# Performance work log

Hardware: AMD Instinct MI355X
Metric: run time of the kernel (lower is better)

The kernel has to match this reference:

```python
import jax, jax.numpy as jnp
import numpy as np

N_USERS = 100000
N_ITEMS = 50000
D = 64
N_LAYERS = 3
E_RAW = 2_000_000
B = 4096


def setup_inputs() -> dict:
    rng = np.random.RandomState(0)
    u = rng.randint(0, N_USERS, E_RAW).astype(np.int64)
    i = rng.randint(0, N_ITEMS, E_RAW).astype(np.int64)
    lin = np.unique(u * N_ITEMS + i)  # dedupe interactions like the dok_matrix would
    u = (lin // N_ITEMS).astype(np.int32)
    i = (lin % N_ITEMS).astype(np.int32)
    deg_u = np.bincount(u, minlength=N_USERS).astype(np.float64)
    deg_i = np.bincount(i, minlength=N_ITEMS).astype(np.float64)
    inv_u = np.where(deg_u > 0, 1.0 / np.sqrt(np.maximum(deg_u, 1.0)), 0.0)
    inv_i = np.where(deg_i > 0, 1.0 / np.sqrt(np.maximum(deg_i, 1.0)), 0.0)
    val = (inv_u[u] * inv_i[i]).astype(np.float32)  # D^-1/2 A D^-1/2 entries
    # symmetric bipartite Laplacian: user block rows then item block rows
    rows = np.concatenate([u, i + N_USERS]).astype(np.int32)
    cols = np.concatenate([i + N_USERS, u]).astype(np.int32)
    vals = np.concatenate([val, val])

    key = jax.random.key(0)
    k1, k2, k3, k4 = jax.random.split(key, 4)
    embeds = jax.random.normal(k1, (N_USERS + N_ITEMS, D), jnp.float32) * 0.1
    users = jax.random.randint(k2, (B,), 0, N_USERS)
    pos_items = jax.random.randint(k3, (B,), 0, N_ITEMS)
    neg_items = jax.random.randint(k4, (B,), 0, N_ITEMS)
    return dict(embeds=embeds, vals=jnp.asarray(vals), rows=jnp.asarray(rows),
                cols=jnp.asarray(cols), users=users, pos_items=pos_items,
                neg_items=neg_items)


def reference(embeds, vals, rows, cols, users, pos_items, neg_items):
    N = N_USERS + N_ITEMS
    cur = embeds
    acc = embeds  # running sum over layer embeddings (incl. layer 0)
    for _ in range(N_LAYERS):
        msg = vals[:, None] * cur[cols]                      # [nnz, D] gather
        cur = jax.ops.segment_sum(msg, rows, num_segments=N)  # SpMM scatter-add
        acc = acc + cur
    mean = acc / (N_LAYERS + 1)
    user_e = mean[:N_USERS]
    item_e = mean[N_USERS:]
    return user_e[users], item_e[pos_items], item_e[neg_items]
```

## Files before the change

### kernel.cpp

```cpp
#include <hip/hip_runtime.h>
#include <hip/hip_bf16.h>

#define N_USERS 100000
#define N_ITEMS 50000
#define N_TOT   150000
#define D       64
#define NBUCK   ((N_ITEMS + 255) >> 8)
#define BCAP    12288
#define CONVU_B 391
#define FLAG_B  48
#define SCAT_K  32

typedef float v2f __attribute__((ext_vector_type(2)));

__device__ __forceinline__ unsigned bf16rn(float f) {
    unsigned x = __float_as_uint(f);
    return (x + 0x7FFFu + ((x >> 16) & 1u)) >> 16;
}
__device__ __forceinline__ unsigned packbf(float a, float b) {
    return bf16rn(a) | (bf16rn(b) << 16);
}
__device__ __forceinline__ int lower_bound(const int* __restrict__ a, int n, int key) {
    int lo = 0, hi = n;
    while (lo < hi) {
        int mid = (lo + hi) >> 1;
        if (a[mid] < key) lo = mid + 1; else hi = mid;
    }
    return lo;
}

__global__ __launch_bounds__(256) void preA_kernel(
        const float* __restrict__ embeds, const int* __restrict__ rows,
        const int* __restrict__ cols, int* __restrict__ user_ptr,
        unsigned* __restrict__ ebfS, float* __restrict__ invrow,
        const int* __restrict__ users, const int* __restrict__ pos,
        const int* __restrict__ neg, unsigned char* __restrict__ flags,
        int* __restrict__ ccur, int* __restrict__ tmp,
        unsigned short* __restrict__ cols16, int E, int B) {
    int b = blockIdx.x, t = threadIdx.x;
    if (b < CONVU_B) {
        __shared__ int ptr_s[257];
        __shared__ float inv_s[256];
        int base = b * 256;
        int r = base + t;
        int v = lower_bound(rows, E, r);
        ptr_s[t] = v;
        if (r <= N_USERS) user_ptr[r] = v;
        if (t == 0) ptr_s[256] = lower_bound(rows, E, base + 256);
        __syncthreads();
        if (r < N_USERS) {
            int deg = ptr_s[t + 1] - ptr_s[t];
            float inv = (deg > 0) ? (float)(1.0 / sqrt((double)deg)) : 0.f;
            inv_s[t] = inv;
            invrow[r] = inv;
        } else inv_s[t] = 0.f;
        __syncthreads();
        int fl = t & 15;
        #pragma unroll
        for (int i = 0; i < 16; ++i) {
            int lr = i * 16 + (t >> 4);
            int row = base + lr;
            if (row < N_USERS) {
                float inv = inv_s[lr];
                float4 v4 = *(const float4*)(embeds + (size_t)row * D + fl * 4);
                uint2 o;
                o.x = packbf(inv * v4.x, inv * v4.y);
                o.y = packbf(inv * v4.z, inv * v4.w);
                *(uint2*)(ebfS + (size_t)row * 32 + fl * 2) = o;
            }
        }
    } else if (b < CONVU_B + FLAG_B) {
        int k = (b - CONVU_B) * 256 + t;
        if (k < 3 * B) {
            int row;
            if (k < B)          row = users[k];
            else if (k < 2 * B) row = N_USERS + pos[k - B];
            else                row = N_USERS + neg[k - 2 * B];
            flags[row] = 1;
        }
    } else {
        __shared__ int ebuf[256 * SCAT_K];
        __shared__ unsigned char bbuf[256 * SCAT_K];
        __shared__ int cnt[NBUCK];
        __shared__ int basep[NBUCK];
        int chunk = (b - CONVU_B - FLAG_B) * (256 * SCAT_K);
        if (t < NBUCK) cnt[t] = 0;
        __syncthreads();
        #pragma unroll 4
        for (int k = 0; k < SCAT_K; ++k) {
            int e = chunk + k * 256 + t;
            int idx = k * 256 + t;
            if (e < E) {
                int i = cols[e] - N_USERS;
                cols16[e] = (unsigned short)i;
                int bu = i >> 8;
                ebuf[idx] = ((i & 255) << 17) | rows[e];
                bbuf[idx] = (unsigned char)bu;
                atomicAdd(&cnt[bu], 1);
            } else bbuf[idx] = 255;
        }
        __syncthreads();
        if (t < NBUCK) {
            int c = cnt[t];
            basep[t] = c ? atomicAdd(&ccur[t], c) : 0;
            cnt[t] = 0;
        }
        __syncthreads();
        #pragma unroll 4
        for (int k = 0; k < SCAT_K; ++k) {
            int idx = k * 256 + t;
            int bu = bbuf[idx];
            if (bu < NBUCK) {
                int pos2 = basep[bu] + atomicAdd(&cnt[bu], 1);
                if (pos2 < BCAP)
                    tmp[(size_t)bu * BCAP + pos2] = ebuf[idx];
            }
        }
    }
}

__global__ __launch_bounds__(256) void preB_kernel(
        const int* __restrict__ tmp, const int* __restrict__ ccur,
        const float* __restrict__ embeds,
        int* __restrict__ item_beg, int* __restrict__ item_end,
        int* __restrict__ nbr, unsigned* __restrict__ ebfS,
        unsigned* __restrict__ bb1, float* __restrict__ invrow) {
    int b = blockIdx.x, t = threadIdx.x;
    if (b == NBUCK) {
        if (t < 16) {
            *(uint2*)(ebfS + (size_t)N_TOT * 32 + t * 2) = make_uint2(0u, 0u);
            *(uint2*)(bb1  + (size_t)N_TOT * 32 + t * 2) = make_uint2(0u, 0u);
        }
        if (t == 0) invrow[N_TOT] = 0.f;
        return;
    }
    __shared__ int stage[BCAP];
    __shared__ int hist[256];
    __shared__ int scn[256];
    __shared__ int curs[256];
    __shared__ float inv_s[256];
    int n = ccur[b]; if (n > BCAP) n = BCAP;
    const int* src = tmp + (size_t)b * BCAP;
    hist[t] = 0;
    __syncthreads();
    for (int p = t; p < n; p += 256) {
        int q = src[p];
        stage[p] = q;
        atomicAdd(&hist[q >> 17], 1);
    }
    __syncthreads();
    scn[t] = hist[t];
    __syncthreads();
    for (int off = 1; off < 256; off <<= 1) {
        int x = (t >= off) ? scn[t - off] : 0;
        __syncthreads();
        scn[t] += x;
        __syncthreads();
    }
    {
        int excl = scn[t] - hist[t];
        curs[t] = excl;
        int gi = (b << 8) + t;
        float inv = (hist[t] > 0) ? (float)(1.0 / sqrt((double)hist[t])) : 0.f;
        inv_s[t] = inv;
        if (gi < N_ITEMS) {
            item_beg[gi] = b * BCAP + excl;
            item_end[gi] = b * BCAP + excl + hist[t];
            invrow[N_USERS + gi] = inv;
        }
    }
    __syncthreads();
    int* dst = nbr + (size_t)b * BCAP;
    for (int p = t; p < n; p += 256) {
        int q = stage[p];
        int pos = atomicAdd(&curs[q >> 17], 1);
        dst[pos] = q & 0x1FFFF;
    }
    int fl = t & 15;
    #pragma unroll
    for (int i = 0; i < 16; ++i) {
        int lr = i * 16 + (t >> 4);
        int gi = (b << 8) + lr;
        if (gi < N_ITEMS) {
            int row = N_USERS + gi;
            float inv = inv_s[lr];
            float4 v4 = *(const float4*)(embeds + (size_t)row * D + fl * 4);
            uint2 o;
            o.x = packbf(inv * v4.x, inv * v4.y);
            o.y = packbf(inv * v4.z, inv * v4.w);
            *(uint2*)(ebfS + (size_t)row * 32 + fl * 2) = o;
        }
    }
}

__global__ __launch_bounds__(256) void agg_kernel(
        const unsigned* __restrict__ gsrc,
        float* __restrict__ nxt, unsigned* __restrict__ nxtb,
        const float* __restrict__ invrow,
        const unsigned char* __restrict__ flags,
        const int* __restrict__ user_ptr, const unsigned short* __restrict__ cols16,
        const int* __restrict__ item_beg, const int* __restrict__ item_end,
        const int* __restrict__ nbr) {
    int wave = (int)((blockIdx.x * blockDim.x + threadIdx.x) >> 6);
    int lane = (int)(threadIdx.x & 63);
    if (wave >= N_TOT) return;
    int g  = lane >> 3;
    int fl = lane & 7;

    bool is_user = wave < N_USERS;
    int s, epos, dummy;
    const unsigned* sb;
    if (is_user) {
        s = user_ptr[wave]; epos = user_ptr[wave + 1];
        sb = gsrc + (size_t)N_USERS * 32; dummy = N_ITEMS;
    } else {
        int i = wave - N_USERS; s = item_beg[i]; epos = item_end[i];
        sb = gsrc; dummy = N_TOT;
    }

    v2f a0 = {0.f, 0.f}, a1 = {0.f, 0.f}, a2 = {0.f, 0.f}, a3 = {0.f, 0.f};

    for (int base = s; base < epos; base += 64) {
        int cnt = epos - base; if (cnt > 64) cnt = 64;
        int col = dummy;
        if (lane < cnt)
            col = is_user ? (int)cols16[base + lane] : nbr[base + lane];
        int tcount = (cnt + 7) >> 3;
        #pragma unroll 4
        for (int t = 0; t < tcount; ++t) {
            int c = __shfl(col, 8 * t + g);
            uint4 q = *(const uint4*)(sb + (size_t)c * 32 + fl * 4);
            v2f p0 = {__uint_as_float(q.x << 16), __uint_as_float(q.x & 0xFFFF0000u)};
            v2f p1 = {__uint_as_float(q.y << 16), __uint_as_float(q.y & 0xFFFF0000u)};
            v2f p2 = {__uint_as_float(q.z << 16), __uint_as_float(q.z & 0xFFFF0000u)};
            v2f p3 = {__uint_as_float(q.w << 16), __uint_as_float(q.w & 0xFFFF0000u)};
            a0 += p0; a1 += p1; a2 += p2; a3 += p3;
        }
    }
    float acc[8] = {a0.x, a0.y, a1.x, a1.y, a2.x, a2.y, a3.x, a3.y};
    #pragma unroll
    for (int j = 0; j < 8; ++j) {
        acc[j] += __shfl_xor(acc[j], 8);
        acc[j] += __shfl_xor(acc[j], 16);
        acc[j] += __shfl_xor(acc[j], 32);
    }
    if (lane < 8) {
        float inv = invrow[wave];
        float f[8];
        #pragma unroll
        for (int j = 0; j < 8; ++j) f[j] = inv * acc[j];
        uint4 o;
        o.x = packbf(inv * f[0], inv * f[1]); o.y = packbf(inv * f[2], inv * f[3]);
        o.z = packbf(inv * f[4], inv * f[5]); o.w = packbf(inv * f[6], inv * f[7]);
        *(uint4*)(nxtb + (size_t)wave * 32 + fl * 4) = o;
        if (flags[wave]) {
            size_t ro = (size_t)wave * D + fl * 8;
            *(float4*)(nxt + ro)     = make_float4(f[0], f[1], f[2], f[3]);
            *(float4*)(nxt + ro + 4) = make_float4(f[4], f[5], f[6], f[7]);
        }
    }
}

__global__ __launch_bounds__(256) void agg3_fused_kernel(
        const unsigned* __restrict__ gsrc,
        const float* __restrict__ e0, const float* __restrict__ e1,
        const float* __restrict__ e2, const float* __restrict__ invrow,
        const int* __restrict__ users, const int* __restrict__ pos,
        const int* __restrict__ neg,
        const int* __restrict__ user_ptr, const unsigned short* __restrict__ cols16,
        const int* __restrict__ item_beg, const int* __restrict__ item_end,
        const int* __restrict__ nbr,
        float* __restrict__ out, int B) {
    int slot = (int)((blockIdx.x * blockDim.x + threadIdx.x) >> 6);
    int lane = (int)(threadIdx.x & 63);
    if (slot >= 3 * B) return;
    int g  = lane >> 3;
    int fl = lane & 7;

    int row;
    if (slot < B)          row = users[slot];
    else if (slot < 2 * B) row = N_USERS + pos[slot - B];
    else                   row = N_USERS + neg[slot - 2 * B];

    bool is_user = row < N_USERS;
    int s, epos, dummy;
    const unsigned* sb;
    if (is_user) {
        s = user_ptr[row]; epos = user_ptr[row + 1];
        sb = gsrc + (size_t)N_USERS * 32; dummy = N_ITEMS;
    } else {
        int i = row - N_USERS; s = item_beg[i]; epos = item_end[i];
        sb = gsrc; dummy = N_TOT;
    }

    v2f a0 = {0.f, 0.f}, a1 = {0.f, 0.f}, a2 = {0.f, 0.f}, a3 = {0.f, 0.f};

    for (int base = s; base < epos; base += 64) {
        int cnt = epos - base; if (cnt > 64) cnt = 64;
        int col = dummy;
        if (lane < cnt)
            col = is_user ? (int)cols16[base + lane] : nbr[base + lane];
        int tcount = (cnt + 7) >> 3;
        #pragma unroll 4
        for (int t = 0; t < tcount; ++t) {
            int c = __shfl(col, 8 * t + g);
            uint4 q = *(const uint4*)(sb + (size_t)c * 32 + fl * 4);
            v2f p0 = {__uint_as_float(q.x << 16), __uint_as_float(q.x & 0xFFFF0000u)};
            v2f p1 = {__uint_as_float(q.y << 16), __uint_as_float(q.y & 0xFFFF0000u)};
            v2f p2 = {__uint_as_float(q.z << 16), __uint_as_float(q.z & 0xFFFF0000u)};
            v2f p3 = {__uint_as_float(q.w << 16), __uint_as_float(q.w & 0xFFFF0000u)};
            a0 += p0; a1 += p1; a2 += p2; a3 += p3;
        }
    }
    float acc[8] = {a0.x, a0.y, a1.x, a1.y, a2.x, a2.y, a3.x, a3.y};
    #pragma unroll
    for (int j = 0; j < 8; ++j) {
        acc[j] += __shfl_xor(acc[j], 8);
        acc[j] += __shfl_xor(acc[j], 16);
        acc[j] += __shfl_xor(acc[j], 32);
    }
    if (lane < 8) {
        float inv = invrow[row];
        size_t ro = (size_t)row * D + fl * 8;
        float4 x0 = *(const float4*)(e0 + ro), x1 = *(const float4*)(e0 + ro + 4);
        float4 y0 = *(const float4*)(e1 + ro), y1 = *(const float4*)(e1 + ro + 4);
        float4 z0 = *(const float4*)(e2 + ro), z1 = *(const float4*)(e2 + ro + 4);
        float4 r0, r1;
        r0.x = (x0.x + y0.x + z0.x + inv * acc[0]) * 0.25f;
        r0.y = (x0.y + y0.y + z0.y + inv * acc[1]) * 0.25f;
        r0.z = (x0.z + y0.z + z0.z + inv * acc[2]) * 0.25f;
        r0.w = (x0.w + y0.w + z0.w + inv * acc[3]) * 0.25f;
        r1.x = (x1.x + y1.x + z1.x + inv * acc[4]) * 0.25f;
        r1.y = (x1.y + y1.y + z1.y + inv * acc[5]) * 0.25f;
        r1.z = (x1.z + y1.z + z1.z + inv * acc[6]) * 0.25f;
        r1.w = (x1.w + y1.w + z1.w + inv * acc[7]) * 0.25f;
        size_t oo = (size_t)slot * D + fl * 8;
        *(float4*)(out + oo)     = r0;
        *(float4*)(out + oo + 4) = r1;
    }
}

extern "C" void kernel_launch(void* const* d_in, const int* in_sizes, int n_in,
                              void* d_out, int out_size, void* d_ws, size_t ws_size,
                              hipStream_t stream) {
    const float* embeds = (const float*)d_in[0];
    const int*   rows   = (const int*)d_in[2];
    const int*   cols   = (const int*)d_in[3];
    const int*   users  = (const int*)d_in[4];
    const int*   pos    = (const int*)d_in[5];
    const int*   neg    = (const int*)d_in[6];
    const int E2 = in_sizes[1];
    const int E  = E2 / 2;
    const int B  = in_sizes[4];

    char* ws = (char*)d_ws;
    size_t off = 0;
    auto alloc = [&](size_t bytes) { void* p = ws + off; off = (off + bytes + 255) & ~(size_t)255; return p; };
    float*    buf1     = (float*)   alloc((size_t)N_TOT * D * sizeof(float));
    float*    buf2     = (float*)   alloc((size_t)N_TOT * D * sizeof(float));
    unsigned* ebfS     = (unsigned*)alloc((size_t)(N_TOT + 1) * 32 * sizeof(unsigned));
    unsigned* bb1      = (unsigned*)alloc((size_t)(N_TOT + 1) * 32 * sizeof(unsigned));
    int*      nbr      = (int*)     alloc((size_t)NBUCK * BCAP * sizeof(int));
    unsigned short* cols16 = (unsigned short*)alloc((size_t)E * sizeof(unsigned short));
    int*      user_ptr = (int*)     alloc((size_t)(N_USERS + 1) * sizeof(int));
    int*      ccur     = (int*)     alloc((size_t)NBUCK * sizeof(int));
    int*      item_beg = (int*)     alloc((size_t)N_ITEMS * sizeof(int));
    int*      item_end = (int*)     alloc((size_t)N_ITEMS * sizeof(int));
    float*    invrow   = (float*)   alloc((size_t)(N_TOT + 1) * sizeof(float));
    unsigned char* flags = (unsigned char*)alloc((size_t)N_TOT);
    int*      tmp      = (int*)buf1;

    hipMemsetAsync(ccur, 0, (size_t)NBUCK * sizeof(int), stream);
    hipMemsetAsync(flags, 0, (size_t)N_TOT, stream);
    const int scatB = (E + 256 * SCAT_K - 1) / (256 * SCAT_K);
    preA_kernel<<<CONVU_B + FLAG_B + scatB, 256, 0, stream>>>(
        embeds, rows, cols, user_ptr, ebfS, invrow, users, pos, neg, flags,
        ccur, tmp, cols16, E, B);
    preB_kernel<<<NBUCK + 1, 256, 0, stream>>>(
        tmp, ccur, embeds, item_beg, item_end, nbr, ebfS, bb1, invrow);

    const int blocks = (N_TOT + 3) / 4;
    agg_kernel<<<blocks, 256, 0, stream>>>(ebfS, buf1, bb1, invrow, flags, user_ptr,
                                           cols16, item_beg, item_end, nbr);
    agg_kernel<<<blocks, 256, 0, stream>>>(bb1, buf2, ebfS, invrow, flags, user_ptr,
                                           cols16, item_beg, item_end, nbr);

    agg3_fused_kernel<<<(3 * B + 3) / 4, 256, 0, stream>>>(
        ebfS, embeds, buf1, buf2, invrow, users, pos, neg,
        user_ptr, cols16, item_beg, item_end, nbr, (float*)d_out, B);
}
```

Measured before the change: 331.3 us.

## Assign agg blocks to user or item work by XCC to localize gathers

Each agg block now takes its work unit from global atomic counters. The choice depends on the XCC it runs on: XCCs with (id>>2)&1==0 take user rows, the others take item rows, and a side that runs out steals from the other counter. The aim is for each XCC's L2 to hold only one side's source embedding table (items for user rows, users for item rows), which should raise cache hit rates on the random gathers. The cost is a per-block atomic, a syncthreads, an extra memset, and an assumption about the XCC-to-half mapping.

New measurement: 1.206 ms. 264% more time.

```diff
diff --git a/kernel.cpp b/kernel.cpp
--- a/kernel.cpp
+++ b/kernel.cpp
@@ -10,6 +10,8 @@
 #define CONVU_B 391
 #define FLAG_B  48
 #define SCAT_K  32
+#define U_UNITS 25000
+#define I_UNITS 12500
 
 typedef float v2f __attribute__((ext_vector_type(2)));
 
@@ -200,21 +202,40 @@
         const unsigned char* __restrict__ flags,
         const int* __restrict__ user_ptr, const unsigned short* __restrict__ cols16,
         const int* __restrict__ item_beg, const int* __restrict__ item_end,
-        const int* __restrict__ nbr) {
-    int wave = (int)((blockIdx.x * blockDim.x + threadIdx.x) >> 6);
+        const int* __restrict__ nbr, int* __restrict__ ctr) {
+    __shared__ int unit_s;
+    if (threadIdx.x == 0) {
+        int xcc;
+        asm volatile("s_getreg_b32 %0, hwreg(HW_REG_XCC_ID)" : "=s"(xcc));
+        int side = (xcc >> 2) & 1;
+        int unit;
+        if (side == 0) {
+            int idx = atomicAdd(&ctr[0], 1);
+            unit = (idx < U_UNITS) ? idx : (U_UNITS + atomicAdd(&ctr[1], 1));
+        } else {
+            int idx = atomicAdd(&ctr[1], 1);
+            unit = (idx < I_UNITS) ? (U_UNITS + idx) : atomicAdd(&ctr[0], 1);
+        }
+        unit_s = unit;
+    }
+    __syncthreads();
+    int unit = unit_s;
+    int lw   = (int)(threadIdx.x >> 6);
     int lane = (int)(threadIdx.x & 63);
-    if (wave >= N_TOT) return;
     int g  = lane >> 3;
     int fl = lane & 7;
 
-    bool is_user = wave < N_USERS;
-    int s, epos, dummy;
+    bool is_user = unit < U_UNITS;
+    int wave, s, epos, dummy;
     const unsigned* sb;
     if (is_user) {
+        wave = unit * 4 + lw;
         s = user_ptr[wave]; epos = user_ptr[wave + 1];
         sb = gsrc + (size_t)N_USERS * 32; dummy = N_ITEMS;
     } else {
-        int i = wave - N_USERS; s = item_beg[i]; epos = item_end[i];
+        int i = (unit - U_UNITS) * 4 + lw;
+        wave = N_USERS + i;
+        s = item_beg[i]; epos = item_end[i];
         sb = gsrc; dummy = N_TOT;
     }
 
@@ -368,10 +389,12 @@
     int*      item_end = (int*)     alloc((size_t)N_ITEMS * sizeof(int));
     float*    invrow   = (float*)   alloc((size_t)(N_TOT + 1) * sizeof(float));
     unsigned char* flags = (unsigned char*)alloc((size_t)N_TOT);
+    int*      ctrs     = (int*)     alloc((size_t)4 * sizeof(int));
     int*      tmp      = (int*)buf1;
 
     hipMemsetAsync(ccur, 0, (size_t)NBUCK * sizeof(int), stream);
     hipMemsetAsync(flags, 0, (size_t)N_TOT, stream);
+    hipMemsetAsync(ctrs, 0, 4 * sizeof(int), stream);
     const int scatB = (E + 256 * SCAT_K - 1) / (256 * SCAT_K);
     preA_kernel<<<CONVU_B + FLAG_B + scatB, 256, 0, stream>>>(
         embeds, rows, cols, user_ptr, ebfS, invrow, users, pos, neg, flags,
@@ -379,11 +402,11 @@
     preB_kernel<<<NBUCK + 1, 256, 0, stream>>>(
         tmp, ccur, embeds, item_beg, item_end, nbr, ebfS, bb1, invrow);
 
-    const int blocks = (N_TOT + 3) / 4;
+    const int blocks = U_UNITS + I_UNITS;
     agg_kernel<<<blocks, 256, 0, stream>>>(ebfS, buf1, bb1, invrow, flags, user_ptr,
-                                           cols16, item_beg, item_end, nbr);
+                                           cols16, item_beg, item_end, nbr, ctrs);
     agg_kernel<<<blocks, 256, 0, stream>>>(bb1, buf2, ebfS, invrow, flags, user_ptr,
-                                           cols16, item_beg, item_end, nbr);
+                                           cols16, item_beg, item_end, nbr, ctrs + 2);
 
     agg3_fused_kernel<<<(3 * B + 3) / 4, 256, 0, stream>>>(
         ebfS, embeds, buf1, buf2, invrow, users, pos, neg,
```

## Build user CSR pointers from row boundaries during scatter; move user conversion to preB

Applied to the files above, without the earlier changes.

The user row pointer array is no longer built by a binary search over the sorted rows array for every user. Instead each edge thread detects boundaries with the next edge and writes user_ptr directly during the scatter pass. The user-embedding conversion to scaled bf16 moves into preB so that it can read the finished pointers. The gather loops in the aggregation kernels are also unrolled 8 instead of 4. This removes about 100k binary searches over 2M entries, at the cost of an extra rows read per edge and moving the conversion blocks into the second kernel.

New measurement: 342.9 us. +3.5%, slower.

```diff
diff --git a/kernel.cpp b/kernel.cpp
--- a/kernel.cpp
+++ b/kernel.cpp
@@ -20,33 +20,91 @@
 __device__ __forceinline__ unsigned packbf(float a, float b) {
     return bf16rn(a) | (bf16rn(b) << 16);
 }
-__device__ __forceinline__ int lower_bound(const int* __restrict__ a, int n, int key) {
-    int lo = 0, hi = n;
-    while (lo < hi) {
-        int mid = (lo + hi) >> 1;
-        if (a[mid] < key) lo = mid + 1; else hi = mid;
-    }
-    return lo;
-}
 
 __global__ __launch_bounds__(256) void preA_kernel(
-        const float* __restrict__ embeds, const int* __restrict__ rows,
-        const int* __restrict__ cols, int* __restrict__ user_ptr,
-        unsigned* __restrict__ ebfS, float* __restrict__ invrow,
+        const int* __restrict__ rows, const int* __restrict__ cols,
+        int* __restrict__ user_ptr,
         const int* __restrict__ users, const int* __restrict__ pos,
         const int* __restrict__ neg, unsigned char* __restrict__ flags,
         int* __restrict__ ccur, int* __restrict__ tmp,
         unsigned short* __restrict__ cols16, int E, int B) {
     int b = blockIdx.x, t = threadIdx.x;
-    if (b < CONVU_B) {
+    if (b < FLAG_B) {
+        int k = b * 256 + t;
+        if (k < 3 * B) {
+            int row;
+            if (k < B)          row = users[k];
+            else if (k < 2 * B) row = N_USERS + pos[k - B];
+            else                row = N_USERS + neg[k - 2 * B];
+            flags[row] = 1;
+        }
+    } else {
+        __shared__ int ebuf[256 * SCAT_K];
+        __shared__ unsigned char bbuf[256 * SCAT_K];
+        __shared__ int cnt[NBUCK];
+        __shared__ int basep[NBUCK];
+        int chunk = (b - FLAG_B) * (256 * SCAT_K);
+        if (t < NBUCK) cnt[t] = 0;
+        __syncthreads();
+        #pragma unroll 4
+        for (int k = 0; k < SCAT_K; ++k) {
+            int e = chunk + k * 256 + t;
+            int idx = k * 256 + t;
+            if (e < E) {
+                int i = cols[e] - N_USERS;
+                int u = rows[e];
+                cols16[e] = (unsigned short)i;
+                int bu = i >> 8;
+                ebuf[idx] = ((i & 255) << 17) | u;
+                bbuf[idx] = (unsigned char)bu;
+                atomicAdd(&cnt[bu], 1);
+                int rnext = (e + 1 < E) ? rows[e + 1] : N_USERS;
+                for (int r = u + 1; r <= rnext; ++r) user_ptr[r] = e + 1;
+                if (e == 0) for (int r = 0; r <= u; ++r) user_ptr[r] = 0;
+            } else bbuf[idx] = 255;
+        }
+        __syncthreads();
+        if (t < NBUCK) {
+            int c = cnt[t];
+            basep[t] = c ? atomicAdd(&ccur[t], c) : 0;
+            cnt[t] = 0;
+        }
+        __syncthreads();
+        #pragma unroll 4
+        for (int k = 0; k < SCAT_K; ++k) {
+            int idx = k * 256 + t;
+            int bu = bbuf[idx];
+            if (bu < NBUCK) {
+                int pos2 = basep[bu] + atomicAdd(&cnt[bu], 1);
+                if (pos2 < BCAP)
+                    tmp[(size_t)bu * BCAP + pos2] = ebuf[idx];
+            }
+        }
+    }
+}
+
+__global__ __launch_bounds__(256) void preB_kernel(
+        const int* __restrict__ tmp, const int* __restrict__ ccur,
+        const float* __restrict__ embeds, const int* __restrict__ user_ptr,
+        int* __restrict__ item_beg, int* __restrict__ item_end,
+        int* __restrict__ nbr, unsigned* __restrict__ ebfS,
+        unsigned* __restrict__ bb1, float* __restrict__ invrow) {
+    int b = blockIdx.x, t = threadIdx.x;
+    if (b >= NBUCK) {
+        if (b == NBUCK + CONVU_B) {
+            if (t < 16) {
+                *(uint2*)(ebfS + (size_t)N_TOT * 32 + t * 2) = make_uint2(0u, 0u);
+                *(uint2*)(bb1  + (size_t)N_TOT * 32 + t * 2) = make_uint2(0u, 0u);
+            }
+            if (t == 0) invrow[N_TOT] = 0.f;
+            return;
+        }
         __shared__ int ptr_s[257];
         __shared__ float inv_s[256];
-        int base = b * 256;
+        int base = (b - NBUCK) * 256;
         int r = base + t;
-        int v = lower_bound(rows, E, r);
-        ptr_s[t] = v;
-        if (r <= N_USERS) user_ptr[r] = v;
-        if (t == 0) ptr_s[256] = lower_bound(rows, E, base + 256);
+        ptr_s[t] = (r <= N_USERS) ? user_ptr[r] : 0;
+        if (t == 0) ptr_s[256] = (base + 256 <= N_USERS) ? user_ptr[base + 256] : 0;
         __syncthreads();
         if (r < N_USERS) {
             int deg = ptr_s[t + 1] - ptr_s[t];
@@ -69,69 +127,6 @@
                 *(uint2*)(ebfS + (size_t)row * 32 + fl * 2) = o;
             }
         }
-    } else if (b < CONVU_B + FLAG_B) {
-        int k = (b - CONVU_B) * 256 + t;
-        if (k < 3 * B) {
-            int row;
-            if (k < B)          row = users[k];
-            else if (k < 2 * B) row = N_USERS + pos[k - B];
-            else                row = N_USERS + neg[k - 2 * B];
-            flags[row] = 1;
-        }
-    } else {
-        __shared__ int ebuf[256 * SCAT_K];
-        __shared__ unsigned char bbuf[256 * SCAT_K];
-        __shared__ int cnt[NBUCK];
-        __shared__ int basep[NBUCK];
-        int chunk = (b - CONVU_B - FLAG_B) * (256 * SCAT_K);
-        if (t < NBUCK) cnt[t] = 0;
-        __syncthreads();
-        #pragma unroll 4
-        for (int k = 0; k < SCAT_K; ++k) {
-            int e = chunk + k * 256 + t;
-            int idx = k * 256 + t;
-            if (e < E) {
-                int i = cols[e] - N_USERS;
-                cols16[e] = (unsigned short)i;
-                int bu = i >> 8;
-                ebuf[idx] = ((i & 255) << 17) | rows[e];
-                bbuf[idx] = (unsigned char)bu;
-                atomicAdd(&cnt[bu], 1);
-            } else bbuf[idx] = 255;
-        }
-        __syncthreads();
-        if (t < NBUCK) {
-            int c = cnt[t];
-            basep[t] = c ? atomicAdd(&ccur[t], c) : 0;
-            cnt[t] = 0;
-        }
-        __syncthreads();
-        #pragma unroll 4
-        for (int k = 0; k < SCAT_K; ++k) {
-            int idx = k * 256 + t;
-            int bu = bbuf[idx];
-            if (bu < NBUCK) {
-                int pos2 = basep[bu] + atomicAdd(&cnt[bu], 1);
-                if (pos2 < BCAP)
-                    tmp[(size_t)bu * BCAP + pos2] = ebuf[idx];
-            }
-        }
-    }
-}
-
-__global__ __launch_bounds__(256) void preB_kernel(
-        const int* __restrict__ tmp, const int* __restrict__ ccur,
-        const float* __restrict__ embeds,
-        int* __restrict__ item_beg, int* __restrict__ item_end,
-        int* __restrict__ nbr, unsigned* __restrict__ ebfS,
-        unsigned* __restrict__ bb1, float* __restrict__ invrow) {
-    int b = blockIdx.x, t = threadIdx.x;
-    if (b == NBUCK) {
-        if (t < 16) {
-            *(uint2*)(ebfS + (size_t)N_TOT * 32 + t * 2) = make_uint2(0u, 0u);
-            *(uint2*)(bb1  + (size_t)N_TOT * 32 + t * 2) = make_uint2(0u, 0u);
-        }
-        if (t == 0) invrow[N_TOT] = 0.f;
         return;
     }
     __shared__ int stage[BCAP];
@@ -226,7 +221,7 @@
         if (lane < cnt)
             col = is_user ? (int)cols16[base + lane] : nbr[base + lane];
         int tcount = (cnt + 7) >> 3;
-        #pragma unroll 4
+        #pragma unroll 8
         for (int t = 0; t < tcount; ++t) {
             int c = __shfl(col, 8 * t + g);
             uint4 q = *(const uint4*)(sb + (size_t)c * 32 + fl * 4);
@@ -301,7 +296,7 @@
         if (lane < cnt)
             col = is_user ? (int)cols16[base + lane] : nbr[base + lane];
         int tcount = (cnt + 7) >> 3;
-        #pragma unroll 4
+        #pragma unroll 8
         for (int t = 0; t < tcount; ++t) {
             int c = __shfl(col, 8 * t + g);
             uint4 q = *(const uint4*)(sb + (size_t)c * 32 + fl * 4);
@@ -373,11 +368,10 @@
     hipMemsetAsync(ccur, 0, (size_t)NBUCK * sizeof(int), stream);
     hipMemsetAsync(flags, 0, (size_t)N_TOT, stream);
     const int scatB = (E + 256 * SCAT_K - 1) / (256 * SCAT_K);
-    preA_kernel<<<CONVU_B + FLAG_B + scatB, 256, 0, stream>>>(
-        embeds, rows, cols, user_ptr, ebfS, invrow, users, pos, neg, flags,
-        ccur, tmp, cols16, E, B);
-    preB_kernel<<<NBUCK + 1, 256, 0, stream>>>(
-        tmp, ccur, embeds, item_beg, item_end, nbr, ebfS, bb1, invrow);
+    preA_kernel<<<FLAG_B + scatB, 256, 0, stream>>>(
+        rows, cols, user_ptr, users, pos, neg, flags, ccur, tmp, cols16, E, B);
+    preB_kernel<<<NBUCK + CONVU_B + 1, 256, 0, stream>>>(
+        tmp, ccur, embeds, user_ptr, item_beg, item_end, nbr, ebfS, bb1, invrow);
 
     const int blocks = (N_TOT + 3) / 4;
     agg_kernel<<<blocks, 256, 0, stream>>>(ebfS, buf1, bb1, invrow, flags, user_ptr,
```
